# Kernel tuning notes

Measured on AMD Instinct MI355X. Metric: run time of the kernel, lower is better.

## Reference

```python
import jax, jax.numpy as jnp
import numpy as np

B, OUT, IN = 1024, 512, 1024

def setup_inputs() -> dict:
    key = jax.random.key(0)
    k1, k2, k3, k4 = jax.random.split(key, 4)
    x = jax.random.uniform(k1, (B, IN), dtype=jnp.float32)            # inputs in [0,1]
    w = jax.random.uniform(k2, (OUT, IN), dtype=jnp.float32)          # centers in [min_input, max_input]=[0,1]
    u = jax.random.uniform(k3, (OUT, IN), dtype=jnp.float32, minval=0.2, maxval=0.7)  # slopes per init
    andor01 = jax.random.randint(k4, (1, OUT), 0, 2).astype(jnp.float32)  # frozen 0/1 mix ('*' mode)
    return {"x": x, "w": w, "u": u, "andor01": andor01}

def reference(x, w, u, andor01):
    # xuw = u * (x[b,None,i] - w[o,i]) ; z[b,o] = sum_i xuw^2 ; y = exp(-z)
    diff = u[None, :, :] * (x[:, None, :] - w[None, :, :])   # [B, OUT, IN]
    z = jnp.sum(diff * diff, axis=-1)                        # [B, OUT]
    y = jnp.exp(-z)                                          # forward of LargeAttractorExp
    # andor == '*': y + andor01 * (1 - 2y)
    return y + andor01 * (1.0 - 2.0 * y)
```

## Files before the change

kernel.cpp:

```cpp
#include <hip/hip_runtime.h>

#define B_SZ   1024
#define OUT_SZ 512
#define IN_SZ  1024
#define NKSTEP 65
#define MT     64
#define NT     32

typedef __bf16 bf16x8 __attribute__((ext_vector_type(8)));
typedef float  f32x4  __attribute__((ext_vector_type(4)));

#define A_ELEMS ((size_t)MT * NKSTEP * 64 * 8)
#define B_ELEMS ((size_t)NT * NKSTEP * 64 * 8)
#define OFF_B   (A_ELEMS * 2)

#define NBLK_A  (MT * NKSTEP / 4)
#define NBLK_B  (NT * NKSTEP / 4)
#define NBLK_R  (OUT_SZ / 4)

__global__ __launch_bounds__(256) void rbf_prep(
    const float* __restrict__ x, const float* __restrict__ w,
    const float* __restrict__ u, __bf16* __restrict__ Ash,
    __bf16* __restrict__ Bsh)
{
    const int blk = blockIdx.x;

    if (blk < NBLK_A) {
        int t = blk * 256 + threadIdx.x;
        int lane  = t & 63;
        int tmp   = t >> 6;
        int kStep = tmp % NKSTEP;
        int mTile = tmp / NKSTEP;
        int b     = mTile * 16 + (lane & 15);
        int quad  = lane >> 4;

        bf16x8 v;
        if (kStep < 64) {
            int kk = kStep * 32 + quad * 8;
            if (kk < IN_SZ) {
                const float4 f0 = *(const float4*)&x[(size_t)b * IN_SZ + kk];
                const float4 f1 = *(const float4*)&x[(size_t)b * IN_SZ + kk + 4];
                float f[8] = {f0.x, f0.y, f0.z, f0.w, f1.x, f1.y, f1.z, f1.w};
                #pragma unroll
                for (int j = 0; j < 8; ++j) v[j] = (__bf16)(f[j] * f[j]);
            } else {
                int i0 = kk - IN_SZ;
                const float4 f0 = *(const float4*)&x[(size_t)b * IN_SZ + i0];
                const float4 f1 = *(const float4*)&x[(size_t)b * IN_SZ + i0 + 4];
                float f[8] = {f0.x, f0.y, f0.z, f0.w, f1.x, f1.y, f1.z, f1.w};
                #pragma unroll
                for (int j = 0; j < 8; ++j) v[j] = (__bf16)f[j];
            }
        } else {
            #pragma unroll
            for (int j = 0; j < 8; ++j) v[j] = (__bf16)0.f;
            if (quad == 0) v[0] = (__bf16)1.f;
        }
        *(bf16x8*)&Ash[(size_t)t * 8] = v;
    } else if (blk < NBLK_A + NBLK_B) {
        int t = (blk - NBLK_A) * 256 + threadIdx.x;
        int lane  = t & 63;
        int tmp   = t >> 6;
        int kStep = tmp % NKSTEP;
        int nTile = tmp / NKSTEP;
        int o     = nTile * 16 + (lane & 15);
        int quad  = lane >> 4;

        bf16x8 v;
        if (kStep < 64) {
            int kk = kStep * 32 + quad * 8;
            if (kk < IN_SZ) {
                const float4 u0 = *(const float4*)&u[(size_t)o * IN_SZ + kk];
                const float4 u1 = *(const float4*)&u[(size_t)o * IN_SZ + kk + 4];
                float uf[8] = {u0.x, u0.y, u0.z, u0.w, u1.x, u1.y, u1.z, u1.w};
                #pragma unroll
                for (int j = 0; j < 8; ++j) v[j] = (__bf16)(uf[j] * uf[j]);
            } else {
                int i0 = kk - IN_SZ;
                const float4 u0 = *(const float4*)&u[(size_t)o * IN_SZ + i0];
                const float4 u1 = *(const float4*)&u[(size_t)o * IN_SZ + i0 + 4];
                const float4 w0 = *(const float4*)&w[(size_t)o * IN_SZ + i0];
                const float4 w1 = *(const float4*)&w[(size_t)o * IN_SZ + i0 + 4];
                float uf[8] = {u0.x, u0.y, u0.z, u0.w, u1.x, u1.y, u1.z, u1.w};
                float wf[8] = {w0.x, w0.y, w0.z, w0.w, w1.x, w1.y, w1.z, w1.w};
                #pragma unroll
                for (int j = 0; j < 8; ++j) v[j] = (__bf16)(-2.f * uf[j] * uf[j] * wf[j]);
            }
            *(bf16x8*)&Bsh[(size_t)t * 8] = v;
        } else if (quad != 0) {
            #pragma unroll
            for (int j = 0; j < 8; ++j) v[j] = (__bf16)0.f;
            *(bf16x8*)&Bsh[(size_t)t * 8] = v;
        }
    } else {
        int wave = threadIdx.x >> 6;
        int lane = threadIdx.x & 63;
        int o    = (blk - NBLK_A - NBLK_B) * 4 + wave;

        float s = 0.f;
        #pragma unroll
        for (int c = 0; c < 4; ++c) {
            int i = lane * 16 + c * 4;
            const float4 uv = *(const float4*)&u[(size_t)o * IN_SZ + i];
            const float4 wv = *(const float4*)&w[(size_t)o * IN_SZ + i];
            float t0 = uv.x * wv.x, t1 = uv.y * wv.y, t2 = uv.z * wv.z, t3 = uv.w * wv.w;
            s += t0 * t0 + t1 * t1 + t2 * t2 + t3 * t3;
        }
        #pragma unroll
        for (int d = 32; d > 0; d >>= 1) s += __shfl_down(s, d);
        if (lane == 0) {
            bf16x8 vr;
            #pragma unroll
            for (int j = 0; j < 8; ++j) vr[j] = (__bf16)0.f;
            vr[0] = (__bf16)s;
            size_t idx = ((size_t)(o >> 4) * NKSTEP + 64) * 64 + (o & 15);
            *(bf16x8*)&Bsh[idx * 8] = vr;
        }
    }
}

__global__ __launch_bounds__(256) void rbf_gemm(
    const __bf16* __restrict__ Ash, const __bf16* __restrict__ Bsh,
    const float* __restrict__ andor, float* __restrict__ out)
{
    const int t    = threadIdx.x;
    const int lane = t & 63;
    const int wv   = t >> 6;
    const int mt2  = wv >> 1;
    const int nt2  = wv & 1;

    const int mTile0 = blockIdx.x * 4 + mt2 * 2;
    const int nTile0 = blockIdx.y * 4 + nt2 * 2;

    f32x4 acc[2][2] = {};

    const __bf16* pa0 = &Ash[(((size_t)mTile0       * NKSTEP) * 64 + lane) * 8];
    const __bf16* pa1 = &Ash[(((size_t)(mTile0 + 1) * NKSTEP) * 64 + lane) * 8];
    const __bf16* pb0 = &Bsh[(((size_t)nTile0       * NKSTEP) * 64 + lane) * 8];
    const __bf16* pb1 = &Bsh[(((size_t)(nTile0 + 1) * NKSTEP) * 64 + lane) * 8];

    #pragma unroll 5
    for (int ks = 0; ks < NKSTEP; ++ks) {
        bf16x8 a0 = *(const bf16x8*)pa0;  pa0 += 64 * 8;
        bf16x8 a1 = *(const bf16x8*)pa1;  pa1 += 64 * 8;
        bf16x8 b0 = *(const bf16x8*)pb0;  pb0 += 64 * 8;
        bf16x8 b1 = *(const bf16x8*)pb1;  pb1 += 64 * 8;
        acc[0][0] = __builtin_amdgcn_mfma_f32_16x16x32_bf16(a0, b0, acc[0][0], 0, 0, 0);
        acc[0][1] = __builtin_amdgcn_mfma_f32_16x16x32_bf16(a0, b1, acc[0][1], 0, 0, 0);
        acc[1][0] = __builtin_amdgcn_mfma_f32_16x16x32_bf16(a1, b0, acc[1][0], 0, 0, 0);
        acc[1][1] = __builtin_amdgcn_mfma_f32_16x16x32_bf16(a1, b1, acc[1][1], 0, 0, 0);
    }

    const int quad = lane >> 4;
    #pragma unroll
    for (int ni = 0; ni < 2; ++ni) {
        int o = (nTile0 + ni) * 16 + (lane & 15);
        float a  = andor[o];
        float s1 = 1.f - 2.f * a;
        #pragma unroll
        for (int mi = 0; mi < 2; ++mi) {
            int b = (mTile0 + mi) * 16 + quad * 4;
            #pragma unroll
            for (int r = 0; r < 4; ++r) {
                float y = __expf(-acc[mi][ni][r]);
                out[(size_t)(b + r) * OUT_SZ + o] = fmaf(y, s1, a);
            }
        }
    }
}

extern "C" void kernel_launch(void* const* d_in, const int* in_sizes, int n_in,
                              void* d_out, int out_size, void* d_ws, size_t ws_size,
                              hipStream_t stream) {
    const float* x = (const float*)d_in[0];
    const float* w = (const float*)d_in[1];
    const float* u = (const float*)d_in[2];
    const float* a = (const float*)d_in[3];
    float* out = (float*)d_out;

    char* ws = (char*)d_ws;
    __bf16* Ash = (__bf16*)ws;
    __bf16* Bsh = (__bf16*)(ws + OFF_B);

    rbf_prep<<<dim3(NBLK_A + NBLK_B + NBLK_R), dim3(256), 0, stream>>>(x, w, u, Ash, Bsh);
    rbf_gemm<<<dim3(B_SZ / 64, OUT_SZ / 64), dim3(256), 0, stream>>>(Ash, Bsh, a, out);
}
```

Measured before the change: 86.57 us.

## Split-K GEMM with LDS double buffering and separate reduce kernel

Drops the 65th K step that carried the ||u*w||^2 bias and keeps that bias in a float buffer instead. The GEMM is split four ways along K, which raises the grid from 128 to 512 blocks. Operand tiles are staged into double-buffered LDS with global_load_lds so the four waves share them. A third kernel sums the partials, adds the bias and applies exp and the and/or mix. The goal is to fill more CUs on the small grid, at the cost of writing and re-reading 8 MB of fp32 partials and one extra launch.

```diff
diff --git a/kernel.cpp b/kernel.cpp
--- a/kernel.cpp
+++ b/kernel.cpp
@@ -3,169 +3,193 @@
 #define B_SZ   1024
 #define OUT_SZ 512
 #define IN_SZ  1024
-#define NKSTEP 65
-#define MT     64
-#define NT     32
+#define NST    64
+#define KSPLIT 4
+#define KPB    (NST / KSPLIT)
+#define CST    4
+#define NCH    (KPB / CST)
 
 typedef __bf16 bf16x8 __attribute__((ext_vector_type(8)));
 typedef float  f32x4  __attribute__((ext_vector_type(4)));
 
-#define A_ELEMS ((size_t)MT * NKSTEP * 64 * 8)
-#define B_ELEMS ((size_t)NT * NKSTEP * 64 * 8)
-#define OFF_B   (A_ELEMS * 2)
-
-#define NBLK_A  (MT * NKSTEP / 4)
-#define NBLK_B  (NT * NKSTEP / 4)
-#define NBLK_R  (OUT_SZ / 4)
+#define APAN_ELEM ((size_t)64 * NST * 64 * 8)
+#define BPAN_ELEM ((size_t)32 * NST * 64 * 8)
+#define OFF_BP   (APAN_ELEM * 2)
+#define OFF_R    (OFF_BP + BPAN_ELEM * 2)
+#define OFF_PART (OFF_R + 8192)
+
+#define NBLK_A 1024
+#define NBLK_B 512
+#define NBLK_R 128
 
 __global__ __launch_bounds__(256) void rbf_prep(
     const float* __restrict__ x, const float* __restrict__ w,
-    const float* __restrict__ u, __bf16* __restrict__ Ash,
-    __bf16* __restrict__ Bsh)
+    const float* __restrict__ u, __bf16* __restrict__ Apan,
+    __bf16* __restrict__ Bpan, float* __restrict__ rbuf)
 {
     const int blk = blockIdx.x;
-
     if (blk < NBLK_A) {
-        int t = blk * 256 + threadIdx.x;
-        int lane  = t & 63;
-        int tmp   = t >> 6;
-        int kStep = tmp % NKSTEP;
-        int mTile = tmp / NKSTEP;
-        int b     = mTile * 16 + (lane & 15);
-        int quad  = lane >> 4;
-
+        int gid  = blk * 256 + threadIdx.x;
+        int lane = gid & 63, unit = gid >> 6;
+        int kStep = unit & 63;
+        int b     = (unit >> 6) * 16 + (lane & 15);
+        int kk    = kStep * 32 + (lane >> 4) * 8;
         bf16x8 v;
-        if (kStep < 64) {
-            int kk = kStep * 32 + quad * 8;
-            if (kk < IN_SZ) {
-                const float4 f0 = *(const float4*)&x[(size_t)b * IN_SZ + kk];
-                const float4 f1 = *(const float4*)&x[(size_t)b * IN_SZ + kk + 4];
-                float f[8] = {f0.x, f0.y, f0.z, f0.w, f1.x, f1.y, f1.z, f1.w};
-                #pragma unroll
-                for (int j = 0; j < 8; ++j) v[j] = (__bf16)(f[j] * f[j]);
-            } else {
-                int i0 = kk - IN_SZ;
-                const float4 f0 = *(const float4*)&x[(size_t)b * IN_SZ + i0];
-                const float4 f1 = *(const float4*)&x[(size_t)b * IN_SZ + i0 + 4];
-                float f[8] = {f0.x, f0.y, f0.z, f0.w, f1.x, f1.y, f1.z, f1.w};
-                #pragma unroll
-                for (int j = 0; j < 8; ++j) v[j] = (__bf16)f[j];
-            }
+        if (kk < IN_SZ) {
+            const float4 f0 = *(const float4*)&x[(size_t)b * IN_SZ + kk];
+            const float4 f1 = *(const float4*)&x[(size_t)b * IN_SZ + kk + 4];
+            float f[8] = {f0.x, f0.y, f0.z, f0.w, f1.x, f1.y, f1.z, f1.w};
+            #pragma unroll
+            for (int j = 0; j < 8; ++j) v[j] = (__bf16)(f[j] * f[j]);
         } else {
-            #pragma unroll
-            for (int j = 0; j < 8; ++j) v[j] = (__bf16)0.f;
-            if (quad == 0) v[0] = (__bf16)1.f;
-        }
-        *(bf16x8*)&Ash[(size_t)t * 8] = v;
+            int i0 = kk - IN_SZ;
+            const float4 f0 = *(const float4*)&x[(size_t)b * IN_SZ + i0];
+            const float4 f1 = *(const float4*)&x[(size_t)b * IN_SZ + i0 + 4];
+            float f[8] = {f0.x, f0.y, f0.z, f0.w, f1.x, f1.y, f1.z, f1.w};
+            #pragma unroll
+            for (int j = 0; j < 8; ++j) v[j] = (__bf16)f[j];
+        }
+        *(bf16x8*)&Apan[(size_t)gid * 8] = v;
     } else if (blk < NBLK_A + NBLK_B) {
-        int t = (blk - NBLK_A) * 256 + threadIdx.x;
-        int lane  = t & 63;
-        int tmp   = t >> 6;
-        int kStep = tmp % NKSTEP;
-        int nTile = tmp / NKSTEP;
-        int o     = nTile * 16 + (lane & 15);
-        int quad  = lane >> 4;
-
+        int gid  = (blk - NBLK_A) * 256 + threadIdx.x;
+        int lane = gid & 63, unit = gid >> 6;
+        int kStep = unit & 63;
+        int o     = (unit >> 6) * 16 + (lane & 15);
+        int kk    = kStep * 32 + (lane >> 4) * 8;
         bf16x8 v;
-        if (kStep < 64) {
-            int kk = kStep * 32 + quad * 8;
-            if (kk < IN_SZ) {
-                const float4 u0 = *(const float4*)&u[(size_t)o * IN_SZ + kk];
-                const float4 u1 = *(const float4*)&u[(size_t)o * IN_SZ + kk + 4];
-                float uf[8] = {u0.x, u0.y, u0.z, u0.w, u1.x, u1.y, u1.z, u1.w};
-                #pragma unroll
-                for (int j = 0; j < 8; ++j) v[j] = (__bf16)(uf[j] * uf[j]);
-            } else {
-                int i0 = kk - IN_SZ;
-                const float4 u0 = *(const float4*)&u[(size_t)o * IN_SZ + i0];
-                const float4 u1 = *(const float4*)&u[(size_t)o * IN_SZ + i0 + 4];
-                const float4 w0 = *(const float4*)&w[(size_t)o * IN_SZ + i0];
-                const float4 w1 = *(const float4*)&w[(size_t)o * IN_SZ + i0 + 4];
-                float uf[8] = {u0.x, u0.y, u0.z, u0.w, u1.x, u1.y, u1.z, u1.w};
-                float wf[8] = {w0.x, w0.y, w0.z, w0.w, w1.x, w1.y, w1.z, w1.w};
-                #pragma unroll
-                for (int j = 0; j < 8; ++j) v[j] = (__bf16)(-2.f * uf[j] * uf[j] * wf[j]);
-            }
-            *(bf16x8*)&Bsh[(size_t)t * 8] = v;
-        } else if (quad != 0) {
-            #pragma unroll
-            for (int j = 0; j < 8; ++j) v[j] = (__bf16)0.f;
-            *(bf16x8*)&Bsh[(size_t)t * 8] = v;
-        }
+        if (kk < IN_SZ) {
+            const float4 u0 = *(const float4*)&u[(size_t)o * IN_SZ + kk];
+            const float4 u1 = *(const float4*)&u[(size_t)o * IN_SZ + kk + 4];
+            float uf[8] = {u0.x, u0.y, u0.z, u0.w, u1.x, u1.y, u1.z, u1.w};
+            #pragma unroll
+            for (int j = 0; j < 8; ++j) v[j] = (__bf16)(uf[j] * uf[j]);
+        } else {
+            int i0 = kk - IN_SZ;
+            const float4 u0 = *(const float4*)&u[(size_t)o * IN_SZ + i0];
+            const float4 u1 = *(const float4*)&u[(size_t)o * IN_SZ + i0 + 4];
+            const float4 w0 = *(const float4*)&w[(size_t)o * IN_SZ + i0];
+            const float4 w1 = *(const float4*)&w[(size_t)o * IN_SZ + i0 + 4];
+            float uf[8] = {u0.x, u0.y, u0.z, u0.w, u1.x, u1.y, u1.z, u1.w};
+            float wf[8] = {w0.x, w0.y, w0.z, w0.w, w1.x, w1.y, w1.z, w1.w};
+            #pragma unroll
+            for (int j = 0; j < 8; ++j) v[j] = (__bf16)(-2.f * uf[j] * uf[j] * wf[j]);
+        }
+        *(bf16x8*)&Bpan[(size_t)gid * 8] = v;
     } else {
-        int wave = threadIdx.x >> 6;
+        int wv   = threadIdx.x >> 6;
         int lane = threadIdx.x & 63;
-        int o    = (blk - NBLK_A - NBLK_B) * 4 + wave;
-
+        int o    = (blk - NBLK_A - NBLK_B) * 4 + wv;
         float s = 0.f;
         #pragma unroll
         for (int c = 0; c < 4; ++c) {
             int i = lane * 16 + c * 4;
             const float4 uv = *(const float4*)&u[(size_t)o * IN_SZ + i];
-            const float4 wv = *(const float4*)&w[(size_t)o * IN_SZ + i];
-            float t0 = uv.x * wv.x, t1 = uv.y * wv.y, t2 = uv.z * wv.z, t3 = uv.w * wv.w;
+            const float4 wv4 = *(const float4*)&w[(size_t)o * IN_SZ + i];
+            float t0 = uv.x * wv4.x, t1 = uv.y * wv4.y, t2 = uv.z * wv4.z, t3 = uv.w * wv4.w;
             s += t0 * t0 + t1 * t1 + t2 * t2 + t3 * t3;
         }
         #pragma unroll
         for (int d = 32; d > 0; d >>= 1) s += __shfl_down(s, d);
-        if (lane == 0) {
-            bf16x8 vr;
-            #pragma unroll
-            for (int j = 0; j < 8; ++j) vr[j] = (__bf16)0.f;
-            vr[0] = (__bf16)s;
-            size_t idx = ((size_t)(o >> 4) * NKSTEP + 64) * 64 + (o & 15);
-            *(bf16x8*)&Bsh[idx * 8] = vr;
-        }
-    }
+        if (lane == 0) rbuf[o] = s;
+    }
+}
+
+__device__ __forceinline__ void ld16_lds(const __bf16* g, __bf16* l) {
+    __builtin_amdgcn_global_load_lds(
+        (const __attribute__((address_space(1))) void*)g,
+        (__attribute__((address_space(3))) void*)l, 16, 0, 0);
 }
 
 __global__ __launch_bounds__(256) void rbf_gemm(
-    const __bf16* __restrict__ Ash, const __bf16* __restrict__ Bsh,
+    const __bf16* __restrict__ Apan, const __bf16* __restrict__ Bpan,
+    float* __restrict__ part)
+{
+    __shared__ __bf16 As[2][16 * 512];
+    __shared__ __bf16 Bs[2][16 * 512];
+
+    const int bid  = blockIdx.x;
+    const int yt   = bid & 7;
+    const int xt   = (bid >> 3) & 15;
+    const int kz   = bid >> 7;
+    const int lane = threadIdx.x & 63;
+    const int wv   = threadIdx.x >> 6;
+    const int wm   = wv >> 1, wn = wv & 1;
+    const int sBase = kz * KPB;
+
+    auto stage = [&](int c, int buf) {
+        const int s0 = sBase + c * CST;
+        #pragma unroll
+        for (int i = 0; i < 8; ++i) {
+            int f = wv * 8 + i;
+            if (f < 16) {
+                int mt = f >> 2, st = f & 3;
+                ld16_lds(&Apan[(((size_t)(xt * 4 + mt) * NST + s0 + st) * 64 + lane) * 8],
+                         &As[buf][(mt * 4 + st) * 512]);
+            } else {
+                int f2 = f - 16;
+                int nt = f2 >> 2, st = f2 & 3;
+                ld16_lds(&Bpan[(((size_t)(yt * 4 + nt) * NST + s0 + st) * 64 + lane) * 8],
+                         &Bs[buf][(nt * 4 + st) * 512]);
+            }
+        }
+    };
+
+    f32x4 acc[2][2] = {};
+
+    stage(0, 0);
+    __syncthreads();
+
+    for (int c = 0; c < NCH; ++c) {
+        const int buf = c & 1;
+        if (c + 1 < NCH) stage(c + 1, buf ^ 1);
+        #pragma unroll
+        for (int st = 0; st < CST; ++st) {
+            bf16x8 a0 = *(const bf16x8*)&As[buf][((wm * 2 + 0) * 4 + st) * 512 + lane * 8];
+            bf16x8 a1 = *(const bf16x8*)&As[buf][((wm * 2 + 1) * 4 + st) * 512 + lane * 8];
+            bf16x8 b0 = *(const bf16x8*)&Bs[buf][((wn * 2 + 0) * 4 + st) * 512 + lane * 8];
+            bf16x8 b1 = *(const bf16x8*)&Bs[buf][((wn * 2 + 1) * 4 + st) * 512 + lane * 8];
+            acc[0][0] = __builtin_amdgcn_mfma_f32_16x16x32_bf16(a0, b0, acc[0][0], 0, 0, 0);
+            acc[0][1] = __builtin_amdgcn_mfma_f32_16x16x32_bf16(a0, b1, acc[0][1], 0, 0, 0);
+            acc[1][0] = __builtin_amdgcn_mfma_f32_16x16x32_bf16(a1, b0, acc[1][0], 0, 0, 0);
+            acc[1][1] = __builtin_amdgcn_mfma_f32_16x16x32_bf16(a1, b1, acc[1][1], 0, 0, 0);
+        }
+        __syncthreads();
+    }
+
+    const int quad = lane >> 4, col = lane & 15;
+    #pragma unroll
+    for (int mi = 0; mi < 2; ++mi) {
+        int b = xt * 64 + (wm * 2 + mi) * 16 + quad * 4;
+        #pragma unroll
+        for (int ni = 0; ni < 2; ++ni) {
+            int o = yt * 64 + (wn * 2 + ni) * 16 + col;
+            #pragma unroll
+            for (int r = 0; r < 4; ++r)
+                part[((size_t)kz * B_SZ + (b + r)) * OUT_SZ + o] = acc[mi][ni][r];
+        }
+    }
+}
+
+__global__ __launch_bounds__(256) void rbf_reduce(
+    const float* __restrict__ part, const float* __restrict__ rbuf,
     const float* __restrict__ andor, float* __restrict__ out)
 {
-    const int t    = threadIdx.x;
-    const int lane = t & 63;
-    const int wv   = t >> 6;
-    const int mt2  = wv >> 1;
-    const int nt2  = wv & 1;
-
-    const int mTile0 = blockIdx.x * 4 + mt2 * 2;
-    const int nTile0 = blockIdx.y * 4 + nt2 * 2;
-
-    f32x4 acc[2][2] = {};
-
-    const __bf16* pa0 = &Ash[(((size_t)mTile0       * NKSTEP) * 64 + lane) * 8];
-    const __bf16* pa1 = &Ash[(((size_t)(mTile0 + 1) * NKSTEP) * 64 + lane) * 8];
-    const __bf16* pb0 = &Bsh[(((size_t)nTile0       * NKSTEP) * 64 + lane) * 8];
-    const __bf16* pb1 = &Bsh[(((size_t)(nTile0 + 1) * NKSTEP) * 64 + lane) * 8];
-
-    #pragma unroll 5
-    for (int ks = 0; ks < NKSTEP; ++ks) {
-        bf16x8 a0 = *(const bf16x8*)pa0;  pa0 += 64 * 8;
-        bf16x8 a1 = *(const bf16x8*)pa1;  pa1 += 64 * 8;
-        bf16x8 b0 = *(const bf16x8*)pb0;  pb0 += 64 * 8;
-        bf16x8 b1 = *(const bf16x8*)pb1;  pb1 += 64 * 8;
-        acc[0][0] = __builtin_amdgcn_mfma_f32_16x16x32_bf16(a0, b0, acc[0][0], 0, 0, 0);
-        acc[0][1] = __builtin_amdgcn_mfma_f32_16x16x32_bf16(a0, b1, acc[0][1], 0, 0, 0);
-        acc[1][0] = __builtin_amdgcn_mfma_f32_16x16x32_bf16(a1, b0, acc[1][0], 0, 0, 0);
-        acc[1][1] = __builtin_amdgcn_mfma_f32_16x16x32_bf16(a1, b1, acc[1][1], 0, 0, 0);
-    }
-
-    const int quad = lane >> 4;
-    #pragma unroll
-    for (int ni = 0; ni < 2; ++ni) {
-        int o = (nTile0 + ni) * 16 + (lane & 15);
-        float a  = andor[o];
-        float s1 = 1.f - 2.f * a;
-        #pragma unroll
-        for (int mi = 0; mi < 2; ++mi) {
-            int b = (mTile0 + mi) * 16 + quad * 4;
-            #pragma unroll
-            for (int r = 0; r < 4; ++r) {
-                float y = __expf(-acc[mi][ni][r]);
-                out[(size_t)(b + r) * OUT_SZ + o] = fmaf(y, s1, a);
-            }
-        }
+    const int base = (blockIdx.x * 256 + threadIdx.x) * 4;
+    if (base < B_SZ * OUT_SZ) {
+        const int ob = base & (OUT_SZ - 1);
+        float4 z = *(const float4*)&rbuf[ob];
+        #pragma unroll
+        for (int kz = 0; kz < KSPLIT; ++kz) {
+            const float4 p = *(const float4*)&part[(size_t)kz * (B_SZ * OUT_SZ) + base];
+            z.x += p.x; z.y += p.y; z.z += p.z; z.w += p.w;
+        }
+        const float4 a = *(const float4*)&andor[ob];
+        float4 o;
+        o.x = fmaf(__expf(-z.x), 1.f - 2.f * a.x, a.x);
+        o.y = fmaf(__expf(-z.y), 1.f - 2.f * a.y, a.y);
+        o.z = fmaf(__expf(-z.z), 1.f - 2.f * a.z, a.z);
+        o.w = fmaf(__expf(-z.w), 1.f - 2.f * a.w, a.w);
+        *(float4*)&out[base] = o;
     }
 }
 
@@ -179,9 +203,12 @@
     float* out = (float*)d_out;
 
     char* ws = (char*)d_ws;
-    __bf16* Ash = (__bf16*)ws;
-    __bf16* Bsh = (__bf16*)(ws + OFF_B);
-
-    rbf_prep<<<dim3(NBLK_A + NBLK_B + NBLK_R), dim3(256), 0, stream>>>(x, w, u, Ash, Bsh);
-    rbf_gemm<<<dim3(B_SZ / 64, OUT_SZ / 64), dim3(256), 0, stream>>>(Ash, Bsh, a, out);
-}
+    __bf16* Apan = (__bf16*)ws;
+    __bf16* Bpan = (__bf16*)(ws + OFF_BP);
+    float*  rbuf = (float*)(ws + OFF_R);
+    float*  part = (float*)(ws + OFF_PART);
+
+    rbf_prep<<<dim3(NBLK_A + NBLK_B + NBLK_R), dim3(256), 0, stream>>>(x, w, u, Apan, Bpan, rbuf);
+    rbf_gemm<<<dim3(16 * 8 * KSPLIT), dim3(256), 0, stream>>>(Apan, Bpan, part);
+    rbf_reduce<<<dim3(B_SZ * OUT_SZ / 4 / 256), dim3(256), 0, stream>>>(part, rbuf, a, out);
+}
```

Measured after the change: 81.91 us. 5.4% less time.
